# Performance work log

Measured on AMD Instinct MI355X. Metric: run time of the kernel, lower is better.

The kernel has to match this reference:

```python
import jax, jax.numpy as jnp
import numpy as np
import math

N_EMB = 768
N_HEAD = 12
N_INNER = 3072
B, T = 2, 2048
EPS = 1e-4


def _gelu_tanh(x):
    return x * 0.5 * (1.0 + jnp.tanh(math.sqrt(2.0 / math.pi) * (x + 0.044715 * x ** 3)))


def _layernorm(x, scale, bias):
    mean = jnp.mean(x, axis=-1, keepdims=True)
    var = jnp.var(x, axis=-1, keepdims=True, ddof=1)  # torch.var default: unbiased
    return scale * ((x - mean) / jnp.sqrt(var + EPS)) + bias


def setup_inputs() -> dict:
    key = jax.random.key(0)
    ks = jax.random.split(key, 16)
    s_attn = 1.0 / math.sqrt(N_EMB)
    s_mlp1 = 1.0 / math.sqrt(N_EMB)
    s_mlp2 = 1.0 / math.sqrt(N_INNER)
    return {
        "x": jax.random.normal(ks[0], (B, T, N_EMB), dtype=jnp.float32),
        "Wq": jax.random.normal(ks[1], (N_EMB, N_EMB), dtype=jnp.float32) * s_attn,
        "bq": jnp.zeros((N_EMB,), jnp.float32),
        "Wk": jax.random.normal(ks[2], (N_EMB, N_EMB), dtype=jnp.float32) * s_attn,
        "bk": jnp.zeros((N_EMB,), jnp.float32),
        "Wv": jax.random.normal(ks[3], (N_EMB, N_EMB), dtype=jnp.float32) * s_attn,
        "bv": jnp.zeros((N_EMB,), jnp.float32),
        "Wo": jax.random.normal(ks[4], (N_EMB, N_EMB), dtype=jnp.float32) * s_attn,
        "bo": jnp.zeros((N_EMB,), jnp.float32),
        "ln1_s": jnp.ones((N_EMB,), jnp.float32),
        "ln1_b": jnp.zeros((N_EMB,), jnp.float32),
        "W1": jax.random.normal(ks[5], (N_EMB, N_INNER), dtype=jnp.float32) * s_mlp1,
        "b1": jnp.zeros((N_INNER,), jnp.float32),
        "W2": jax.random.normal(ks[6], (N_INNER, N_EMB), dtype=jnp.float32) * s_mlp2,
        "b2": jnp.zeros((N_EMB,), jnp.float32),
        "ln2_s": jnp.ones((N_EMB,), jnp.float32),
        "ln2_b": jnp.zeros((N_EMB,), jnp.float32),
    }


def reference(x, Wq, bq, Wk, bk, Wv, bv, Wo, bo, ln1_s, ln1_b, W1, b1, W2, b2, ln2_s, ln2_b):
    Bx, Tx, C = x.shape
    dh = C // N_HEAD
    # QKV projections -> [B, H, T, dh]
    def split_heads(y):
        return y.reshape(Bx, Tx, N_HEAD, dh).transpose(0, 2, 1, 3)
    q = split_heads(x @ Wq + bq)
    k = split_heads(x @ Wk + bk)
    v = split_heads(x @ Wv + bv)
    # naive full-score causal attention (materializes [B,H,T,T])
    scores = jnp.einsum("bhqd,bhkd->bhqk", q, k)
    causal = jnp.tril(jnp.ones((Tx, Tx), dtype=bool))
    scores = jnp.where(causal, scores, -jnp.inf)
    attn = jax.nn.softmax(scores / math.sqrt(dh), axis=-1)
    ctx = jnp.einsum("bhqk,bhkd->bhqd", attn, v)
    ctx = ctx.transpose(0, 2, 1, 3).reshape(Bx, Tx, C)
    attn_out = ctx @ Wo + bo
    # post-norm residual
    h = _layernorm(x + attn_out, ln1_s, ln1_b)
    mlp_out = _gelu_tanh(h @ W1 + b1) @ W2 + b2
    return _layernorm(h + mlp_out, ln2_s, ln2_b)
```

## Files before the change

### kernel.cpp

```cpp
#include <hip/hip_runtime.h>
#include <math.h>

#define TB  2
#define TT  2048
#define TC  768
#define TH  12
#define TDH 64
#define TI  3072
#define TM  (TB*TT)

typedef __attribute__((ext_vector_type(8))) __bf16 bf16x8;
typedef __attribute__((ext_vector_type(4))) __bf16 bf16x4;
typedef __attribute__((ext_vector_type(4))) float  f32x4;

__device__ __forceinline__ float gelu_tanh(float x) {
    float x3 = x * x * x;
    return 0.5f * x * (1.0f + tanhf(0.7978845608028654f * (x + 0.044715f * x3)));
}

__device__ __forceinline__ void gld_lds16(const void* g, void* l) {
    __builtin_amdgcn_global_load_lds(
        (const __attribute__((address_space(1))) unsigned int*)g,
        (__attribute__((address_space(3))) unsigned int*)l,
        16, 0, 0);
}

#define BK 32

template<int BM_, int BN_, int WM_, int WN_>
__global__ __launch_bounds__(256)
void gemm_mfma(const __bf16* __restrict__ A, const __bf16* __restrict__ Bt,
               const float* __restrict__ b0, const float* __restrict__ b1,
               const float* __restrict__ b2, const float* __restrict__ resid,
               float* __restrict__ outf, __bf16* __restrict__ outb,
               int N, int K, size_t wt_stride, size_t out_stride, int ep)
{
    constexpr int WAVES_N = BN_ / WN_;
    constexpr int TMt = WM_ / 16, TNt = WN_ / 16;
    constexpr int AISS = BM_ / 64, BISS = BN_ / 64;
    constexpr int TILE = (BM_ + BN_) * BK;
    __shared__ __align__(16) __bf16 lds[2 * TILE];

    const int tid  = threadIdx.x;
    const int wave = tid >> 6, lane = tid & 63;
    const int wm = wave / WAVES_N, wn = wave % WAVES_N;
    const int m0 = blockIdx.y * BM_, n0 = blockIdx.x * BN_;
    const int z  = blockIdx.z;

    const __bf16* Bz = Bt + (size_t)z * wt_stride;
    const size_t Kb = (size_t)K * 2;
    const char* Ag = (const char*)A + (size_t)m0 * Kb;
    const char* Bg = (const char*)Bz + (size_t)n0 * Kb;
    const int srow = tid >> 2;
    const int scol = ((tid & 3) ^ ((tid >> 4) & 3)) * 16;
    const int wbase = wave * 1024;

    f32x4 acc[TMt][TNt];
    #pragma unroll
    for (int i = 0; i < TMt; ++i)
        #pragma unroll
        for (int j = 0; j < TNt; ++j)
            acc[i][j] = (f32x4){0.f, 0.f, 0.f, 0.f};

    const int arow = wm * WM_ + (lane & 15);
    const int brow = wn * WN_ + (lane & 15);
    const int koff = (((lane >> 4) ^ ((lane >> 2) & 3))) * 8;

    const int nIter = K / BK;

    auto stage = [&](int buf, int k0b) {
        char* base = (char*)lds + (size_t)buf * TILE * 2;
        #pragma unroll
        for (int s = 0; s < AISS; ++s)
            gld_lds16(Ag + (size_t)(srow + 64 * s) * Kb + k0b + scol,
                      base + s * 4096 + wbase);
        char* bbase = base + BM_ * BK * 2;
        #pragma unroll
        for (int s = 0; s < BISS; ++s)
            gld_lds16(Bg + (size_t)(srow + 64 * s) * Kb + k0b + scol,
                      bbase + s * 4096 + wbase);
    };

    stage(0, 0);
    int buf = 0;
    for (int it = 0; it < nIter; ++it) {
        __syncthreads();
        if (it + 1 < nIter) stage(buf ^ 1, (it + 1) * (BK * 2));

        const __bf16* As = lds + (size_t)buf * TILE;
        const __bf16* Bs = As + BM_ * BK;
        bf16x8 af[TMt], bfr[TNt];
        #pragma unroll
        for (int ti = 0; ti < TMt; ++ti)
            af[ti] = *(const bf16x8*)&As[(arow + ti * 16) * BK + koff];
        #pragma unroll
        for (int tj = 0; tj < TNt; ++tj)
            bfr[tj] = *(const bf16x8*)&Bs[(brow + tj * 16) * BK + koff];
        #pragma unroll
        for (int ti = 0; ti < TMt; ++ti)
            #pragma unroll
            for (int tj = 0; tj < TNt; ++tj)
                acc[ti][tj] = __builtin_amdgcn_mfma_f32_16x16x32_bf16(
                    af[ti], bfr[tj], acc[ti][tj], 0, 0, 0);
        buf ^= 1;
    }

    const int lrow = m0 + wm * WM_ + ((lane >> 4) << 2);
    const int lcol = n0 + wn * WN_ + (lane & 15);

    if (ep == 0) {
        const float* bias = (z == 0) ? b0 : (z == 1) ? b1 : b2;
        __bf16* outz = outb + (size_t)z * out_stride;
        if (z < 2) {
            #pragma unroll
            for (int tj = 0; tj < TNt; ++tj) {
                int n = lcol + tj * 16;
                float bj = bias[n];
                int h = n >> 6, d = n & 63;
                #pragma unroll
                for (int ti = 0; ti < TMt; ++ti)
                    #pragma unroll
                    for (int r = 0; r < 4; ++r) {
                        int m = lrow + ti * 16 + r;
                        int b = m >> 11, t = m & (TT - 1);
                        outz[((size_t)(b * TH + h) * TT + t) * TDH + d] =
                            (__bf16)(acc[ti][tj][r] + bj);
                    }
            }
        } else {
            #pragma unroll
            for (int tj = 0; tj < TNt; ++tj) {
                int n = lcol + tj * 16;
                float bj = bias[n];
                int h = n >> 6, d = n & 63;
                #pragma unroll
                for (int ti = 0; ti < TMt; ++ti) {
                    int m = lrow + ti * 16;
                    int b = m >> 11, t0 = m & (TT - 1);
                    bf16x4 pk;
                    #pragma unroll
                    for (int r = 0; r < 4; ++r)
                        pk[r] = (__bf16)(acc[ti][tj][r] + bj);
                    *(bf16x4*)(outz + ((size_t)(b * TH + h) * TDH + d) * TT + t0) = pk;
                }
            }
        }
    } else if (ep == 1) {
        #pragma unroll
        for (int tj = 0; tj < TNt; ++tj) {
            int n = lcol + tj * 16;
            float bj = b0[n];
            #pragma unroll
            for (int ti = 0; ti < TMt; ++ti)
                #pragma unroll
                for (int r = 0; r < 4; ++r) {
                    int m = lrow + ti * 16 + r;
                    outf[(size_t)m * N + n] =
                        acc[ti][tj][r] + bj + resid[(size_t)m * N + n];
                }
        }
    } else {
        #pragma unroll
        for (int tj = 0; tj < TNt; ++tj) {
            int n = lcol + tj * 16;
            float bj = b0[n];
            #pragma unroll
            for (int ti = 0; ti < TMt; ++ti)
                #pragma unroll
                for (int r = 0; r < 4; ++r) {
                    int m = lrow + ti * 16 + r;
                    outb[(size_t)m * N + n] = (__bf16)gelu_tanh(acc[ti][tj][r] + bj);
                }
        }
    }
}

__global__ __launch_bounds__(256)
void prep_kernel(const float* __restrict__ x,
                 const float* __restrict__ Wq, const float* __restrict__ Wk,
                 const float* __restrict__ Wv, const float* __restrict__ Wo,
                 const float* __restrict__ W1, const float* __restrict__ W2,
                 __bf16* __restrict__ x_bf, __bf16* __restrict__ WqkvT,
                 __bf16* __restrict__ WoT, __bf16* __restrict__ W1T,
                 __bf16* __restrict__ W2T)
{
    const size_t WSZ = (size_t)TC * TC;
    int bid = blockIdx.x;
    if (bid < 1536) {
        int i = (bid * 256 + threadIdx.x) * 8;
        float4 a = *(const float4*)(x + i);
        float4 b = *(const float4*)(x + i + 4);
        bf16x8 v;
        v[0] = (__bf16)a.x; v[1] = (__bf16)a.y; v[2] = (__bf16)a.z; v[3] = (__bf16)a.w;
        v[4] = (__bf16)b.x; v[5] = (__bf16)b.y; v[6] = (__bf16)b.z; v[7] = (__bf16)b.w;
        *(bf16x8*)(x_bf + i) = v;
        return;
    }
    bid -= 1536;
    const float* src; __bf16* dst; int K, N, tloc;
    if (bid < 2304) {
        int w = bid / 576; tloc = bid - w * 576;
        K = TC; N = TC;
        src = (w == 0) ? Wq : (w == 1) ? Wk : (w == 2) ? Wv : Wo;
        dst = (w < 3) ? (WqkvT + (size_t)w * WSZ) : WoT;
    } else if (bid < 4608) {
        tloc = bid - 2304; K = TC; N = TI; src = W1; dst = W1T;
    } else {
        tloc = bid - 4608; K = TI; N = TC; src = W2; dst = W2T;
    }
    int tiles_x = N >> 5;
    int n0 = (tloc % tiles_x) * 32, k0 = (tloc / tiles_x) * 32;

    __shared__ float tile[32][33];
    const int tx = threadIdx.x & 31, ty = threadIdx.x >> 5;
    #pragma unroll
    for (int i = 0; i < 32; i += 8)
        tile[ty + i][tx] = src[(size_t)(k0 + ty + i) * N + n0 + tx];
    __syncthreads();
    #pragma unroll
    for (int i = 0; i < 32; i += 8)
        dst[(size_t)(n0 + ty + i) * K + k0 + tx] = (__bf16)tile[tx][ty + i];
}

__global__ __launch_bounds__(256)
void ln_kernel(const float* __restrict__ in, const float* __restrict__ gs,
               const float* __restrict__ gb, float* __restrict__ out,
               __bf16* __restrict__ out_bf)
{
    const int row = blockIdx.x, tid = threadIdx.x;
    const float* r = in + (size_t)row * TC;
    float x0 = r[tid], x1 = r[tid + 256], x2 = r[tid + 512];
    float s = x0 + x1 + x2;
    float q = x0 * x0 + x1 * x1 + x2 * x2;
    #pragma unroll
    for (int off = 32; off > 0; off >>= 1) {
        s += __shfl_down(s, off);
        q += __shfl_down(q, off);
    }
    __shared__ float partial[8];
    __shared__ float stats[2];
    int wid = tid >> 6, lane = tid & 63;
    if (lane == 0) { partial[wid] = s; partial[wid + 4] = q; }
    __syncthreads();
    if (tid == 0) {
        float S = partial[0] + partial[1] + partial[2] + partial[3];
        float Q = partial[4] + partial[5] + partial[6] + partial[7];
        float mean = S * (1.0f / (float)TC);
        float var = (Q - (float)TC * mean * mean) * (1.0f / (float)(TC - 1));
        stats[0] = mean;
        stats[1] = rsqrtf(var + 1e-4f);
    }
    __syncthreads();
    float mean = stats[0], rstd = stats[1];
    float* w = out + (size_t)row * TC;
    float y0 = gs[tid]       * ((x0 - mean) * rstd) + gb[tid];
    float y1 = gs[tid + 256] * ((x1 - mean) * rstd) + gb[tid + 256];
    float y2 = gs[tid + 512] * ((x2 - mean) * rstd) + gb[tid + 512];
    w[tid] = y0; w[tid + 256] = y1; w[tid + 512] = y2;
    if (out_bf) {
        __bf16* wb = out_bf + (size_t)row * TC;
        wb[tid] = (__bf16)y0; wb[tid + 256] = (__bf16)y1; wb[tid + 512] = (__bf16)y2;
    }
}

#define AP 72

__global__ __launch_bounds__(256)
void attn_mfma(const __bf16* __restrict__ Q, const __bf16* __restrict__ K,
               const __bf16* __restrict__ Vt, __bf16* __restrict__ ctx)
{
    __shared__ __align__(16) __bf16 Ks[64 * AP];
    __shared__ __align__(16) __bf16 Vs[64 * AP];
    __shared__ __align__(16) __bf16 Ps[64 * AP];

    const int tid  = threadIdx.x;
    const int wave = tid >> 6, lane = tid & 63;
    const int c = lane & 15, g = lane >> 4;
    const int bh = blockIdx.y;
    const int qi = blockIdx.x;
    const int qt = (qi & 1) ? (31 - (qi >> 1)) : (qi >> 1);
    const int q_glob = qt * 64 + wave * 16 + c;

    const __bf16* Qb = Q  + (size_t)bh * TT * TDH;
    const __bf16* Kb = K  + (size_t)bh * TT * TDH;
    const __bf16* Vb = Vt + (size_t)bh * TDH * TT;

    bf16x8 qf0 = *(const bf16x8*)(Qb + (size_t)q_glob * TDH + g * 8);
    bf16x8 qf1 = *(const bf16x8*)(Qb + (size_t)q_glob * TDH + 32 + g * 8);

    const int srow = tid >> 3;
    const int sc   = (tid & 7) * 8;

    float m_i = -1e30f, l_i = 0.0f;
    f32x4 acc[4];
    #pragma unroll
    for (int m2 = 0; m2 < 4; ++m2) acc[m2] = (f32x4){0.f, 0.f, 0.f, 0.f};

    for (int kt = 0; kt <= qt; ++kt) {
        bf16x8 kv0 = *(const bf16x8*)(Kb + (size_t)(kt * 64 + srow) * TDH + sc);
        bf16x8 kv1 = *(const bf16x8*)(Kb + (size_t)(kt * 64 + srow + 32) * TDH + sc);
        bf16x8 vv0 = *(const bf16x8*)(Vb + (size_t)srow * TT + kt * 64 + sc);
        bf16x8 vv1 = *(const bf16x8*)(Vb + (size_t)(srow + 32) * TT + kt * 64 + sc);
        __syncthreads();
        *(bf16x8*)&Ks[srow * AP + sc]        = kv0;
        *(bf16x8*)&Ks[(srow + 32) * AP + sc] = kv1;
        *(bf16x8*)&Vs[srow * AP + sc]        = vv0;
        *(bf16x8*)&Vs[(srow + 32) * AP + sc] = vv1;
        __syncthreads();

        f32x4 st[4];
        #pragma unroll
        for (int g2 = 0; g2 < 4; ++g2) {
            bf16x8 af0 = *(const bf16x8*)&Ks[(16 * g2 + c) * AP + g * 8];
            bf16x8 af1 = *(const bf16x8*)&Ks[(16 * g2 + c) * AP + 32 + g * 8];
            f32x4 z = (f32x4){0.f, 0.f, 0.f, 0.f};
            z = __builtin_amdgcn_mfma_f32_16x16x32_bf16(af0, qf0, z, 0, 0, 0);
            z = __builtin_amdgcn_mfma_f32_16x16x32_bf16(af1, qf1, z, 0, 0, 0);
            st[g2] = z;
        }

        float sv[4][4];
        float mx = -1e30f;
        if (kt == qt) {
            #pragma unroll
            for (int g2 = 0; g2 < 4; ++g2)
                #pragma unroll
                for (int r = 0; r < 4; ++r) {
                    int kcol = kt * 64 + 16 * g2 + 4 * g + r;
                    float v = (kcol > q_glob) ? -1e30f : st[g2][r] * 0.125f;
                    sv[g2][r] = v;
                    mx = fmaxf(mx, v);
                }
        } else {
            #pragma unroll
            for (int g2 = 0; g2 < 4; ++g2)
                #pragma unroll
                for (int r = 0; r < 4; ++r) {
                    float v = st[g2][r] * 0.125f;
                    sv[g2][r] = v;
                    mx = fmaxf(mx, v);
                }
        }
        mx = fmaxf(mx, __shfl_xor(mx, 16));
        mx = fmaxf(mx, __shfl_xor(mx, 32));
        float nm = fmaxf(m_i, mx);
        float corr = __expf(m_i - nm);
        float ps = 0.f;
        #pragma unroll
        for (int g2 = 0; g2 < 4; ++g2) {
            bf16x4 pk;
            #pragma unroll
            for (int r = 0; r < 4; ++r) {
                float p = __expf(sv[g2][r] - nm);
                ps += p;
                pk[r] = (__bf16)p;
            }
            *(bf16x4*)&Ps[(wave * 16 + c) * AP + 16 * g2 + 4 * g] = pk;
        }
        ps += __shfl_xor(ps, 16);
        ps += __shfl_xor(ps, 32);
        l_i = l_i * corr + ps;
        m_i = nm;
        #pragma unroll
        for (int m2 = 0; m2 < 4; ++m2) {
            acc[m2][0] *= corr; acc[m2][1] *= corr;
            acc[m2][2] *= corr; acc[m2][3] *= corr;
        }

        bf16x8 pf0 = *(const bf16x8*)&Ps[(wave * 16 + c) * AP + g * 8];
        bf16x8 pf1 = *(const bf16x8*)&Ps[(wave * 16 + c) * AP + 32 + g * 8];
        #pragma unroll
        for (int m2 = 0; m2 < 4; ++m2) {
            bf16x8 vf0 = *(const bf16x8*)&Vs[(16 * m2 + c) * AP + g * 8];
            bf16x8 vf1 = *(const bf16x8*)&Vs[(16 * m2 + c) * AP + 32 + g * 8];
            acc[m2] = __builtin_amdgcn_mfma_f32_16x16x32_bf16(vf0, pf0, acc[m2], 0, 0, 0);
            acc[m2] = __builtin_amdgcn_mfma_f32_16x16x32_bf16(vf1, pf1, acc[m2], 0, 0, 0);
        }
    }

    const int b = bh / TH, h = bh - b * TH;
    float inv = 1.0f / l_i;
    #pragma unroll
    for (int m2 = 0; m2 < 4; ++m2) {
        bf16x4 o;
        #pragma unroll
        for (int r = 0; r < 4; ++r)
            o[r] = (__bf16)(acc[m2][r] * inv);
        *(bf16x4*)(ctx + ((size_t)b * TT + q_glob) * TC + h * TDH + 16 * m2 + 4 * g) = o;
    }
}

extern "C" void kernel_launch(void* const* d_in, const int* in_sizes, int n_in,
                              void* d_out, int out_size, void* d_ws, size_t ws_size,
                              hipStream_t stream)
{
    const float* x    = (const float*)d_in[0];
    const float* Wq   = (const float*)d_in[1];
    const float* bq   = (const float*)d_in[2];
    const float* Wk   = (const float*)d_in[3];
    const float* bk   = (const float*)d_in[4];
    const float* Wv   = (const float*)d_in[5];
    const float* bv   = (const float*)d_in[6];
    const float* Wo   = (const float*)d_in[7];
    const float* bo   = (const float*)d_in[8];
    const float* ln1s = (const float*)d_in[9];
    const float* ln1b = (const float*)d_in[10];
    const float* W1   = (const float*)d_in[11];
    const float* b1   = (const float*)d_in[12];
    const float* W2   = (const float*)d_in[13];
    const float* b2   = (const float*)d_in[14];
    const float* ln2s = (const float*)d_in[15];
    const float* ln2b = (const float*)d_in[16];
    float* out = (float*)d_out;

    const size_t MC  = (size_t)TM * TC;
    const size_t MCB = MC * 2;
    const size_t WSZ = (size_t)TC * TC;
    const size_t W12 = (size_t)TC * TI;

    char* W = (char*)d_ws;
    __bf16* qkvb  = (__bf16*)W;
    __bf16* x_bf  = (__bf16*)(W + 3 * MCB);
    float*  tmp1  = (float*)W;
    __bf16* u_bf  = (__bf16*)W;
    float*  h_f32 = (float*)(W + 4 * MCB);
    __bf16* ctxh  = (__bf16*)(W + 6 * MCB);
    __bf16* wts   = (__bf16*)(W + 7 * MCB);
    __bf16* WqkvT = wts;
    __bf16* WoT   = WqkvT + 3 * WSZ;
    __bf16* W1T   = WoT + WSZ;
    __bf16* W2T   = W1T + W12;

    dim3 blk(256);

    prep_kernel<<<dim3(1536 + 6912), blk, 0, stream>>>(
        x, Wq, Wk, Wv, Wo, W1, W2, x_bf, WqkvT, WoT, W1T, W2T);

    gemm_mfma<128, 128, 64, 64><<<dim3(TC / 128, TM / 128, 3), blk, 0, stream>>>(
        x_bf, WqkvT, bq, bk, bv, nullptr, nullptr, qkvb, TC, TC, WSZ, MC, 0);

    attn_mfma<<<dim3(TT / 64, TB * TH), blk, 0, stream>>>(
        qkvb, qkvb + MC, qkvb + 2 * MC, ctxh);

    gemm_mfma<64, 128, 32, 64><<<dim3(TC / 128, TM / 64, 1), blk, 0, stream>>>(
        ctxh, WoT, bo, nullptr, nullptr, x, tmp1, nullptr, TC, TC, 0, 0, 1);

    ln_kernel<<<dim3(TM), blk, 0, stream>>>(tmp1, ln1s, ln1b, h_f32, ctxh);

    gemm_mfma<128, 128, 64, 64><<<dim3(TI / 128, TM / 128, 1), blk, 0, stream>>>(
        ctxh, W1T, b1, nullptr, nullptr, nullptr, nullptr, u_bf, TI, TC, 0, 0, 2);

    gemm_mfma<64, 128, 32, 64><<<dim3(TC / 128, TM / 64, 1), blk, 0, stream>>>(
        u_bf, W2T, b2, nullptr, nullptr, h_f32, out, nullptr, TC, TI, 0, 0, 1);

    ln_kernel<<<dim3(TM), blk, 0, stream>>>(out, ln2s, ln2b, out, nullptr);
}
```

Measured before the change: 323.5 us.

## Double-buffer K/V tiles in attention, use exp2 softmax, remap blocks

The attention kernel now double-buffers its K/V shared-memory tiles. The next tile's global loads are issued before the current tile's MFMAs, and the data is written to the alternate buffer afterwards, which removes one barrier per iteration and overlaps load latency with compute. Softmax switches to exp2f with the log2(e) factor folded into the scale, and MFMA sections are wrapped in s_setprio. Block indices are remapped so neighbouring blocks land on different heads, which should spread the causal load imbalance. The cost is double the K/V LDS footprint and more registers held across the loop, which may reduce occupancy.

```diff
diff --git a/kernel.cpp b/kernel.cpp
--- a/kernel.cpp
+++ b/kernel.cpp
@@ -264,20 +264,24 @@
 }
 
 #define AP 72
+#define ATT_SCALE 0.18033688011112042f
 
 __global__ __launch_bounds__(256)
 void attn_mfma(const __bf16* __restrict__ Q, const __bf16* __restrict__ K,
                const __bf16* __restrict__ Vt, __bf16* __restrict__ ctx)
 {
-    __shared__ __align__(16) __bf16 Ks[64 * AP];
-    __shared__ __align__(16) __bf16 Vs[64 * AP];
+    __shared__ __align__(16) __bf16 Ks[2][64 * AP];
+    __shared__ __align__(16) __bf16 Vs[2][64 * AP];
     __shared__ __align__(16) __bf16 Ps[64 * AP];
 
     const int tid  = threadIdx.x;
     const int wave = tid >> 6, lane = tid & 63;
     const int c = lane & 15, g = lane >> 4;
-    const int bh = blockIdx.y;
-    const int qi = blockIdx.x;
+
+    const int r8 = blockIdx.x & 7, jj = blockIdx.x >> 3;
+    const int ii = blockIdx.y * 4 + jj;
+    const int bh = r8 * 3 + (ii >> 5);
+    const int qi = ii & 31;
     const int qt = (qi & 1) ? (31 - (qi >> 1)) : (qi >> 1);
     const int q_glob = qt * 64 + wave * 16 + c;
 
@@ -296,28 +300,46 @@
     #pragma unroll
     for (int m2 = 0; m2 < 4; ++m2) acc[m2] = (f32x4){0.f, 0.f, 0.f, 0.f};
 
+    {
+        bf16x8 kv0 = *(const bf16x8*)(Kb + (size_t)srow * TDH + sc);
+        bf16x8 kv1 = *(const bf16x8*)(Kb + (size_t)(srow + 32) * TDH + sc);
+        bf16x8 vv0 = *(const bf16x8*)(Vb + (size_t)srow * TT + sc);
+        bf16x8 vv1 = *(const bf16x8*)(Vb + (size_t)(srow + 32) * TT + sc);
+        *(bf16x8*)&Ks[0][srow * AP + sc]        = kv0;
+        *(bf16x8*)&Ks[0][(srow + 32) * AP + sc] = kv1;
+        *(bf16x8*)&Vs[0][srow * AP + sc]        = vv0;
+        *(bf16x8*)&Vs[0][(srow + 32) * AP + sc] = vv1;
+    }
+    __syncthreads();
+
     for (int kt = 0; kt <= qt; ++kt) {
-        bf16x8 kv0 = *(const bf16x8*)(Kb + (size_t)(kt * 64 + srow) * TDH + sc);
-        bf16x8 kv1 = *(const bf16x8*)(Kb + (size_t)(kt * 64 + srow + 32) * TDH + sc);
-        bf16x8 vv0 = *(const bf16x8*)(Vb + (size_t)srow * TT + kt * 64 + sc);
-        bf16x8 vv1 = *(const bf16x8*)(Vb + (size_t)(srow + 32) * TT + kt * 64 + sc);
-        __syncthreads();
-        *(bf16x8*)&Ks[srow * AP + sc]        = kv0;
-        *(bf16x8*)&Ks[(srow + 32) * AP + sc] = kv1;
-        *(bf16x8*)&Vs[srow * AP + sc]        = vv0;
-        *(bf16x8*)&Vs[(srow + 32) * AP + sc] = vv1;
-        __syncthreads();
+        const int cur = kt & 1;
+        const bool pre = (kt < qt);
+
+        bf16x8 kv0, kv1, vv0, vv1;
+        if (pre) {
+            const int kb = (kt + 1) * 64;
+            kv0 = *(const bf16x8*)(Kb + (size_t)(kb + srow) * TDH + sc);
+            kv1 = *(const bf16x8*)(Kb + (size_t)(kb + srow + 32) * TDH + sc);
+            vv0 = *(const bf16x8*)(Vb + (size_t)srow * TT + kb + sc);
+            vv1 = *(const bf16x8*)(Vb + (size_t)(srow + 32) * TT + kb + sc);
+        }
+
+        const __bf16* Kc = Ks[cur];
+        const __bf16* Vc = Vs[cur];
 
         f32x4 st[4];
+        __builtin_amdgcn_s_setprio(1);
         #pragma unroll
         for (int g2 = 0; g2 < 4; ++g2) {
-            bf16x8 af0 = *(const bf16x8*)&Ks[(16 * g2 + c) * AP + g * 8];
-            bf16x8 af1 = *(const bf16x8*)&Ks[(16 * g2 + c) * AP + 32 + g * 8];
+            bf16x8 af0 = *(const bf16x8*)&Kc[(16 * g2 + c) * AP + g * 8];
+            bf16x8 af1 = *(const bf16x8*)&Kc[(16 * g2 + c) * AP + 32 + g * 8];
             f32x4 z = (f32x4){0.f, 0.f, 0.f, 0.f};
             z = __builtin_amdgcn_mfma_f32_16x16x32_bf16(af0, qf0, z, 0, 0, 0);
             z = __builtin_amdgcn_mfma_f32_16x16x32_bf16(af1, qf1, z, 0, 0, 0);
             st[g2] = z;
         }
+        __builtin_amdgcn_s_setprio(0);
 
         float sv[4][4];
         float mx = -1e30f;
@@ -327,7 +349,7 @@
                 #pragma unroll
                 for (int r = 0; r < 4; ++r) {
                     int kcol = kt * 64 + 16 * g2 + 4 * g + r;
-                    float v = (kcol > q_glob) ? -1e30f : st[g2][r] * 0.125f;
+                    float v = (kcol > q_glob) ? -1e30f : st[g2][r] * ATT_SCALE;
                     sv[g2][r] = v;
                     mx = fmaxf(mx, v);
                 }
@@ -336,7 +358,7 @@
             for (int g2 = 0; g2 < 4; ++g2)
                 #pragma unroll
                 for (int r = 0; r < 4; ++r) {
-                    float v = st[g2][r] * 0.125f;
+                    float v = st[g2][r] * ATT_SCALE;
                     sv[g2][r] = v;
                     mx = fmaxf(mx, v);
                 }
@@ -344,14 +366,14 @@
         mx = fmaxf(mx, __shfl_xor(mx, 16));
         mx = fmaxf(mx, __shfl_xor(mx, 32));
         float nm = fmaxf(m_i, mx);
-        float corr = __expf(m_i - nm);
+        float corr = exp2f(m_i - nm);
         float ps = 0.f;
         #pragma unroll
         for (int g2 = 0; g2 < 4; ++g2) {
             bf16x4 pk;
             #pragma unroll
             for (int r = 0; r < 4; ++r) {
-                float p = __expf(sv[g2][r] - nm);
+                float p = exp2f(sv[g2][r] - nm);
                 ps += p;
                 pk[r] = (__bf16)p;
             }
@@ -369,13 +391,24 @@
 
         bf16x8 pf0 = *(const bf16x8*)&Ps[(wave * 16 + c) * AP + g * 8];
         bf16x8 pf1 = *(const bf16x8*)&Ps[(wave * 16 + c) * AP + 32 + g * 8];
+        __builtin_amdgcn_s_setprio(1);
         #pragma unroll
         for (int m2 = 0; m2 < 4; ++m2) {
-            bf16x8 vf0 = *(const bf16x8*)&Vs[(16 * m2 + c) * AP + g * 8];
-            bf16x8 vf1 = *(const bf16x8*)&Vs[(16 * m2 + c) * AP + 32 + g * 8];
+            bf16x8 vf0 = *(const bf16x8*)&Vc[(16 * m2 + c) * AP + g * 8];
+            bf16x8 vf1 = *(const bf16x8*)&Vc[(16 * m2 + c) * AP + 32 + g * 8];
             acc[m2] = __builtin_amdgcn_mfma_f32_16x16x32_bf16(vf0, pf0, acc[m2], 0, 0, 0);
             acc[m2] = __builtin_amdgcn_mfma_f32_16x16x32_bf16(vf1, pf1, acc[m2], 0, 0, 0);
         }
+        __builtin_amdgcn_s_setprio(0);
+
+        if (pre) {
+            const int nb = cur ^ 1;
+            *(bf16x8*)&Ks[nb][srow * AP + sc]        = kv0;
+            *(bf16x8*)&Ks[nb][(srow + 32) * AP + sc] = kv1;
+            *(bf16x8*)&Vs[nb][srow * AP + sc]        = vv0;
+            *(bf16x8*)&Vs[nb][(srow + 32) * AP + sc] = vv1;
+        }
+        __syncthreads();
     }
 
     const int b = bh / TH, h = bh - b * TH;
```

Measured after the change: 325.6 us. About the same (+0.6%).

## Persist attention blocks with balanced jobs and double-buffered async K/V loads

Applied to the files above, without the earlier changes.

The attention kernel becomes a persistent grid of 256 blocks. Each block handles three (query-tile, head) jobs, chosen so that short and long causal rows are paired for balance. K/V tiles are now loaded with global_load_lds into double-buffered, XOR-swizzled LDS, so the next tile's fetch overlaps the current tile's MFMA work, with one barrier per iteration. Softmax uses exp2f with log2(e) folded into the scale. The trade-off is fewer resident blocks per CU, so latency hiding across blocks is reduced, and the kernel now depends on a hard-coded job mapping.

```diff
diff --git a/kernel.cpp b/kernel.cpp
--- a/kernel.cpp
+++ b/kernel.cpp
@@ -264,129 +264,155 @@
 }
 
 #define AP 72
+#define ATT_SCALE 0.18033688011112042f
 
 __global__ __launch_bounds__(256)
 void attn_mfma(const __bf16* __restrict__ Q, const __bf16* __restrict__ K,
                const __bf16* __restrict__ Vt, __bf16* __restrict__ ctx)
 {
-    __shared__ __align__(16) __bf16 Ks[64 * AP];
-    __shared__ __align__(16) __bf16 Vs[64 * AP];
+    __shared__ __align__(16) __bf16 Ks[2][64 * 64];
+    __shared__ __align__(16) __bf16 Vs[2][64 * 64];
     __shared__ __align__(16) __bf16 Ps[64 * AP];
 
     const int tid  = threadIdx.x;
     const int wave = tid >> 6, lane = tid & 63;
     const int c = lane & 15, g = lane >> 4;
-    const int bh = blockIdx.y;
-    const int qi = blockIdx.x;
-    const int qt = (qi & 1) ? (31 - (qi >> 1)) : (qi >> 1);
-    const int q_glob = qt * 64 + wave * 16 + c;
-
-    const __bf16* Qb = Q  + (size_t)bh * TT * TDH;
-    const __bf16* Kb = K  + (size_t)bh * TT * TDH;
-    const __bf16* Vb = Vt + (size_t)bh * TDH * TT;
-
-    bf16x8 qf0 = *(const bf16x8*)(Qb + (size_t)q_glob * TDH + g * 8);
-    bf16x8 qf1 = *(const bf16x8*)(Qb + (size_t)q_glob * TDH + 32 + g * 8);
-
-    const int srow = tid >> 3;
-    const int sc   = (tid & 7) * 8;
-
-    float m_i = -1e30f, l_i = 0.0f;
-    f32x4 acc[4];
-    #pragma unroll
-    for (int m2 = 0; m2 < 4; ++m2) acc[m2] = (f32x4){0.f, 0.f, 0.f, 0.f};
-
-    for (int kt = 0; kt <= qt; ++kt) {
-        bf16x8 kv0 = *(const bf16x8*)(Kb + (size_t)(kt * 64 + srow) * TDH + sc);
-        bf16x8 kv1 = *(const bf16x8*)(Kb + (size_t)(kt * 64 + srow + 32) * TDH + sc);
-        bf16x8 vv0 = *(const bf16x8*)(Vb + (size_t)srow * TT + kt * 64 + sc);
-        bf16x8 vv1 = *(const bf16x8*)(Vb + (size_t)(srow + 32) * TT + kt * 64 + sc);
+    const int blk = blockIdx.x;
+
+    const int r8   = tid >> 3;
+    const int swz  = ((tid & 7) ^ ((tid >> 3) & 7)) * 16;
+    const int ldsw = wave * 1024;
+
+    const int x0 = ((g    ) ^ (c & 7)) * 16;
+    const int x1 = ((g + 4) ^ (c & 7)) * 16;
+
+    int jobs[3];
+    jobs[0] = blk;
+    { int q0 = blk / 24, h0 = blk - (blk / 24) * 24; jobs[1] = (31 - q0) * 24 + h0; }
+    jobs[2] = (blk < 248) ? (256 + blk) : (520 + (blk - 248));
+
+    for (int jj = 0; jj < 3; ++jj) {
+        const int p  = jobs[jj];
+        const int qt = p / 24, bh = p - (p / 24) * 24;
+        const int q_glob = qt * 64 + wave * 16 + c;
+
+        const __bf16* Qb = Q + (size_t)bh * TT * TDH;
+        const char*   Kg = (const char*)(K  + (size_t)bh * TT * TDH);
+        const char*   Vg = (const char*)(Vt + (size_t)bh * TDH * TT);
+
+        bf16x8 qf0 = *(const bf16x8*)(Qb + (size_t)q_glob * TDH + g * 8);
+        bf16x8 qf1 = *(const bf16x8*)(Qb + (size_t)q_glob * TDH + 32 + g * 8);
+
+        float m_i = -1e30f, l_i = 0.0f;
+        f32x4 acc[4];
+        #pragma unroll
+        for (int m2 = 0; m2 < 4; ++m2) acc[m2] = (f32x4){0.f, 0.f, 0.f, 0.f};
+
+        auto stage = [&](int buf, int kt) {
+            const char* kg = Kg + (size_t)(kt * 64 + r8) * 128 + swz;
+            const char* vg = Vg + (size_t)r8 * (TT * 2) + kt * 128 + swz;
+            char* kl = (char*)&Ks[buf][0] + ldsw;
+            char* vl = (char*)&Vs[buf][0] + ldsw;
+            gld_lds16(kg,                  kl);
+            gld_lds16(kg + 32 * 128,       kl + 4096);
+            gld_lds16(vg,                  vl);
+            gld_lds16(vg + 32 * (TT * 2),  vl + 4096);
+        };
+
+        stage(0, 0);
         __syncthreads();
-        *(bf16x8*)&Ks[srow * AP + sc]        = kv0;
-        *(bf16x8*)&Ks[(srow + 32) * AP + sc] = kv1;
-        *(bf16x8*)&Vs[srow * AP + sc]        = vv0;
-        *(bf16x8*)&Vs[(srow + 32) * AP + sc] = vv1;
-        __syncthreads();
-
-        f32x4 st[4];
-        #pragma unroll
-        for (int g2 = 0; g2 < 4; ++g2) {
-            bf16x8 af0 = *(const bf16x8*)&Ks[(16 * g2 + c) * AP + g * 8];
-            bf16x8 af1 = *(const bf16x8*)&Ks[(16 * g2 + c) * AP + 32 + g * 8];
-            f32x4 z = (f32x4){0.f, 0.f, 0.f, 0.f};
-            z = __builtin_amdgcn_mfma_f32_16x16x32_bf16(af0, qf0, z, 0, 0, 0);
-            z = __builtin_amdgcn_mfma_f32_16x16x32_bf16(af1, qf1, z, 0, 0, 0);
-            st[g2] = z;
+
+        for (int kt = 0; kt <= qt; ++kt) {
+            const int cur = kt & 1;
+            if (kt < qt) stage(cur ^ 1, kt + 1);
+
+            const char* Kc = (const char*)&Ks[cur][0];
+            const char* Vc = (const char*)&Vs[cur][0];
+
+            f32x4 st[4];
+            #pragma unroll
+            for (int g2 = 0; g2 < 4; ++g2) {
+                const int row = (16 * g2 + c) * 128;
+                bf16x8 af0 = *(const bf16x8*)(Kc + row + x0);
+                bf16x8 af1 = *(const bf16x8*)(Kc + row + x1);
+                f32x4 z = (f32x4){0.f, 0.f, 0.f, 0.f};
+                z = __builtin_amdgcn_mfma_f32_16x16x32_bf16(af0, qf0, z, 0, 0, 0);
+                z = __builtin_amdgcn_mfma_f32_16x16x32_bf16(af1, qf1, z, 0, 0, 0);
+                st[g2] = z;
+            }
+
+            float sv[4][4];
+            float mx = -1e30f;
+            if (kt == qt) {
+                #pragma unroll
+                for (int g2 = 0; g2 < 4; ++g2)
+                    #pragma unroll
+                    for (int r = 0; r < 4; ++r) {
+                        int kcol = kt * 64 + 16 * g2 + 4 * g + r;
+                        float v = (kcol > q_glob) ? -1e30f : st[g2][r] * ATT_SCALE;
+                        sv[g2][r] = v;
+                        mx = fmaxf(mx, v);
+                    }
+            } else {
+                #pragma unroll
+                for (int g2 = 0; g2 < 4; ++g2)
+                    #pragma unroll
+                    for (int r = 0; r < 4; ++r) {
+                        float v = st[g2][r] * ATT_SCALE;
+                        sv[g2][r] = v;
+                        mx = fmaxf(mx, v);
+                    }
+            }
+            mx = fmaxf(mx, __shfl_xor(mx, 16));
+            mx = fmaxf(mx, __shfl_xor(mx, 32));
+            float nm = fmaxf(m_i, mx);
+            float corr = exp2f(m_i - nm);
+            float ps = 0.f;
+            #pragma unroll
+            for (int g2 = 0; g2 < 4; ++g2) {
+                bf16x4 pk;
+                #pragma unroll
+                for (int r = 0; r < 4; ++r) {
+                    float pp = exp2f(sv[g2][r] - nm);
+                    ps += pp;
+                    pk[r] = (__bf16)pp;
+                }
+                *(bf16x4*)&Ps[(wave * 16 + c) * AP + 16 * g2 + 4 * g] = pk;
+            }
+            ps += __shfl_xor(ps, 16);
+            ps += __shfl_xor(ps, 32);
+            l_i = l_i * corr + ps;
+            m_i = nm;
+            #pragma unroll
+            for (int m2 = 0; m2 < 4; ++m2) {
+                acc[m2][0] *= corr; acc[m2][1] *= corr;
+                acc[m2][2] *= corr; acc[m2][3] *= corr;
+            }
+
+            bf16x8 pf0 = *(const bf16x8*)&Ps[(wave * 16 + c) * AP + g * 8];
+            bf16x8 pf1 = *(const bf16x8*)&Ps[(wave * 16 + c) * AP + 32 + g * 8];
+            #pragma unroll
+            for (int m2 = 0; m2 < 4; ++m2) {
+                const int vrow = (16 * m2 + c) * 128;
+                bf16x8 vf0 = *(const bf16x8*)(Vc + vrow + x0);
+                bf16x8 vf1 = *(const bf16x8*)(Vc + vrow + x1);
+                acc[m2] = __builtin_amdgcn_mfma_f32_16x16x32_bf16(vf0, pf0, acc[m2], 0, 0, 0);
+                acc[m2] = __builtin_amdgcn_mfma_f32_16x16x32_bf16(vf1, pf1, acc[m2], 0, 0, 0);
+            }
+
+            __syncthreads();
         }
 
-        float sv[4][4];
-        float mx = -1e30f;
-        if (kt == qt) {
-            #pragma unroll
-            for (int g2 = 0; g2 < 4; ++g2)
-                #pragma unroll
-                for (int r = 0; r < 4; ++r) {
-                    int kcol = kt * 64 + 16 * g2 + 4 * g + r;
-                    float v = (kcol > q_glob) ? -1e30f : st[g2][r] * 0.125f;
-                    sv[g2][r] = v;
-                    mx = fmaxf(mx, v);
-                }
-        } else {
-            #pragma unroll
-            for (int g2 = 0; g2 < 4; ++g2)
-                #pragma unroll
-                for (int r = 0; r < 4; ++r) {
-                    float v = st[g2][r] * 0.125f;
-                    sv[g2][r] = v;
-                    mx = fmaxf(mx, v);
-                }
+        const int b = bh / TH, h = bh - b * TH;
+        float inv = 1.0f / l_i;
+        #pragma unroll
+        for (int m2 = 0; m2 < 4; ++m2) {
+            bf16x4 o;
+            #pragma unroll
+            for (int r = 0; r < 4; ++r)
+                o[r] = (__bf16)(acc[m2][r] * inv);
+            *(bf16x4*)(ctx + ((size_t)b * TT + q_glob) * TC + h * TDH + 16 * m2 + 4 * g) = o;
         }
-        mx = fmaxf(mx, __shfl_xor(mx, 16));
-        mx = fmaxf(mx, __shfl_xor(mx, 32));
-        float nm = fmaxf(m_i, mx);
-        float corr = __expf(m_i - nm);
-        float ps = 0.f;
-        #pragma unroll
-        for (int g2 = 0; g2 < 4; ++g2) {
-            bf16x4 pk;
-            #pragma unroll
-            for (int r = 0; r < 4; ++r) {
-                float p = __expf(sv[g2][r] - nm);
-                ps += p;
-                pk[r] = (__bf16)p;
-            }
-            *(bf16x4*)&Ps[(wave * 16 + c) * AP + 16 * g2 + 4 * g] = pk;
-        }
-        ps += __shfl_xor(ps, 16);
-        ps += __shfl_xor(ps, 32);
-        l_i = l_i * corr + ps;
-        m_i = nm;
-        #pragma unroll
-        for (int m2 = 0; m2 < 4; ++m2) {
-            acc[m2][0] *= corr; acc[m2][1] *= corr;
-            acc[m2][2] *= corr; acc[m2][3] *= corr;
-        }
-
-        bf16x8 pf0 = *(const bf16x8*)&Ps[(wave * 16 + c) * AP + g * 8];
-        bf16x8 pf1 = *(const bf16x8*)&Ps[(wave * 16 + c) * AP + 32 + g * 8];
-        #pragma unroll
-        for (int m2 = 0; m2 < 4; ++m2) {
-            bf16x8 vf0 = *(const bf16x8*)&Vs[(16 * m2 + c) * AP + g * 8];
-            bf16x8 vf1 = *(const bf16x8*)&Vs[(16 * m2 + c) * AP + 32 + g * 8];
-            acc[m2] = __builtin_amdgcn_mfma_f32_16x16x32_bf16(vf0, pf0, acc[m2], 0, 0, 0);
-            acc[m2] = __builtin_amdgcn_mfma_f32_16x16x32_bf16(vf1, pf1, acc[m2], 0, 0, 0);
-        }
-    }
-
-    const int b = bh / TH, h = bh - b * TH;
-    float inv = 1.0f / l_i;
-    #pragma unroll
-    for (int m2 = 0; m2 < 4; ++m2) {
-        bf16x4 o;
-        #pragma unroll
-        for (int r = 0; r < 4; ++r)
-            o[r] = (__bf16)(acc[m2][r] * inv);
-        *(bf16x4*)(ctx + ((size_t)b * TT + q_glob) * TC + h * TDH + 16 * m2 + 4 * g) = o;
     }
 }
 
@@ -439,7 +465,7 @@
     gemm_mfma<128, 128, 64, 64><<<dim3(TC / 128, TM / 128, 3), blk, 0, stream>>>(
         x_bf, WqkvT, bq, bk, bv, nullptr, nullptr, qkvb, TC, TC, WSZ, MC, 0);
 
-    attn_mfma<<<dim3(TT / 64, TB * TH), blk, 0, stream>>>(
+    attn_mfma<<<dim3(256), blk, 0, stream>>>(
         qkvb, qkvb + MC, qkvb + 2 * MC, ctxh);
 
     gemm_mfma<64, 128, 32, 64><<<dim3(TC / 128, TM / 64, 1), blk, 0, stream>>>(
```

Measured after the change: 331.5 us. 1.02x slower.
